# Performance work log

Measured on AMD Instinct MI355X. Metric: run time of the kernel, lower is better.

Reference implementation:

```python
import jax, jax.numpy as jnp
import numpy as np
from jax.scipy.linalg import expm

B, T, D = 4096, 256, 64


def setup_inputs() -> dict:
    key = jax.random.key(0)
    k1, k2, k3 = jax.random.split(key, 3)
    inputs = jax.random.normal(k1, (B, T, D), dtype=jnp.float32)
    time = jax.random.uniform(k2, (T,), dtype=jnp.float32)  # TIME grid in [0,1)
    kernel = jax.random.normal(k3, (D, D), dtype=jnp.float32) * 0.1  # learned Koopman generator
    return {"inputs": inputs, "time": time, "kernel": kernel}


def reference(inputs, time, kernel):
    # expm(kernel * t) for every t, batched instead of a Python loop: [T, D, D]
    mats = jax.vmap(lambda t: expm(kernel * t))(time)
    # original: einsum('ijk,lk->lij', mats, inputs[:, 0, :]) -> [B, T, D]
    x0 = inputs[:, 0, :]  # [B, D] initial condition
    trajs = jnp.einsum('tij,bj->bti', mats, x0)
    return trajs
```

## Files before the change

kernel.cpp:

```cpp
#include <hip/hip_runtime.h>
#include <math.h>


#define TT 256
#define DD 64
#define BB 4096
#define S1 68
#define THETA 0.5f
#define MTERMS 10

__device__ __forceinline__ void mm68(const float* __restrict__ Lt,
                                     const float* __restrict__ R,
                                     float* __restrict__ C,
                                     float f, float* __restrict__ Eacc, int tid) {
    const int i0 = (tid & 15) * 4;
    const int j0 = (tid >> 4) * 4;
    float acc[4][4];
#pragma unroll
    for (int r = 0; r < 4; ++r)
#pragma unroll
        for (int c = 0; c < 4; ++c) acc[r][c] = 0.f;

#pragma unroll 8
    for (int k = 0; k < 64; ++k) {
        const float4 a = *reinterpret_cast<const float4*>(&Lt[k * S1 + i0]);
        const float4 b = *reinterpret_cast<const float4*>(&R[k * S1 + j0]);
        const float av[4] = {a.x, a.y, a.z, a.w};
        const float bv[4] = {b.x, b.y, b.z, b.w};
#pragma unroll
        for (int r = 0; r < 4; ++r)
#pragma unroll
            for (int c = 0; c < 4; ++c) acc[r][c] = fmaf(av[r], bv[c], acc[r][c]);
    }

#pragma unroll
    for (int r = 0; r < 4; ++r) {
        float4 v;
        v.x = acc[r][0] * f; v.y = acc[r][1] * f; v.z = acc[r][2] * f; v.w = acc[r][3] * f;
        *reinterpret_cast<float4*>(&C[(i0 + r) * S1 + j0]) = v;
        if (Eacc) {
            float* e = &Eacc[(i0 + r) * S1 + j0];
            e[0] += v.x; e[1] += v.y; e[2] += v.z; e[3] += v.w;
        }
    }
}

__device__ __forceinline__ void transpose68(const float* __restrict__ X,
                                            float* __restrict__ XT, int tid) {
    const int i = tid >> 2;
    const int j0 = (tid & 3) * 16;
#pragma unroll
    for (int c4 = 0; c4 < 4; ++c4) {
        const float4 v = *reinterpret_cast<const float4*>(&X[i * S1 + j0 + 4 * c4]);
        XT[(j0 + 4 * c4 + 0) * S1 + i] = v.x;
        XT[(j0 + 4 * c4 + 1) * S1 + i] = v.y;
        XT[(j0 + 4 * c4 + 2) * S1 + i] = v.z;
        XT[(j0 + 4 * c4 + 3) * S1 + i] = v.w;
    }
}

__global__ __launch_bounds__(256)
void expm_kernel(const float* __restrict__ K, const float* __restrict__ tim,
                 float* __restrict__ G) {
    __shared__ float As[64 * S1];
    __shared__ float Pa[64 * S1];
    __shared__ float Pb[64 * S1];
    __shared__ float Et[64 * S1];
    __shared__ float Tx[64 * S1];
    __shared__ float red[64];

    const int tid = threadIdx.x;
    const int t = blockIdx.x;
    const float tval = tim[t];

    if (tid < 64) {
        float s = 0.f;
        for (int j = 0; j < 64; ++j) s += fabsf(K[tid * 64 + j]);
        red[tid] = s;
    }
    __syncthreads();
    if (tid == 0) {
        float m = 0.f;
        for (int i = 0; i < 64; ++i) m = fmaxf(m, red[i]);
        const float nt = m * tval;
        int s = 0;
        if (nt > THETA) {
            s = (int)ceilf(log2f(nt / THETA));
            if (s < 0) s = 0;
        }
        red[0] = ldexpf(tval, -s);
        red[1] = (float)s;
    }
    __syncthreads();
    const float scale = red[0];
    const int sq = (int)red[1];
    __syncthreads();

    {
        const int i = tid >> 2;
        const int j0 = (tid & 3) * 16;
#pragma unroll
        for (int c = 0; c < 16; ++c) {
            const int j = j0 + c;
            const float v = K[i * 64 + j] * scale;
            As[i * S1 + j] = v;
            Pa[j * S1 + i] = v;
            Et[j * S1 + i] = v + ((i == j) ? 1.f : 0.f);
        }
    }
    __syncthreads();

    float* Pcur = Pa;
    float* Pnext = Pb;
    for (int n = 2; n <= MTERMS; ++n) {
        mm68(As, Pcur, Pnext, 1.0f / (float)n, Et, tid);
        __syncthreads();
        float* tmp = Pcur; Pcur = Pnext; Pnext = tmp;
    }

    transpose68(Et, Tx, tid);
    __syncthreads();
    float* cur = Tx;
    float* nxt = Pa;
    const float* curT = Et;
    for (int r = 0; r < sq; ++r) {
        if (r > 0) {
            transpose68(cur, Pb, tid);
            __syncthreads();
            curT = Pb;
        }
        mm68(curT, cur, nxt, 1.f, nullptr, tid);
        __syncthreads();
        float* tmp = cur; cur = nxt; nxt = tmp;
    }

    {
        const int j = tid >> 2;
        const int i0 = (tid & 3) * 16;
        float* outp = G + (size_t)t * 4096 + j * 64 + i0;
#pragma unroll
        for (int c4 = 0; c4 < 4; ++c4) {
            float4 v;
            v.x = cur[(i0 + 4 * c4 + 0) * S1 + j];
            v.y = cur[(i0 + 4 * c4 + 1) * S1 + j];
            v.z = cur[(i0 + 4 * c4 + 2) * S1 + j];
            v.w = cur[(i0 + 4 * c4 + 3) * S1 + j];
            *reinterpret_cast<float4*>(outp + 4 * c4) = v;
        }
    }
}

__global__ __launch_bounds__(256)
void traj_kernel(const float* __restrict__ inputs, const float* __restrict__ G,
                 float* __restrict__ out) {
    __shared__ float MT[64 * 64];
    __shared__ float X0T[64 * S1];

    const int tid = threadIdx.x;
    const int t = blockIdx.x & (TT - 1);
    const int b0 = (blockIdx.x >> 8) * 64;

    {
        const float4* src = reinterpret_cast<const float4*>(G) + (size_t)t * 1024;
        float4* dst = reinterpret_cast<float4*>(MT);
#pragma unroll
        for (int c = 0; c < 4; ++c) dst[tid + 256 * c] = src[tid + 256 * c];
    }
    {
        const int bb = tid >> 2;
        const int j0 = (tid & 3) * 16;
        const float* src = inputs + (size_t)(b0 + bb) * (TT * DD) + j0;
#pragma unroll
        for (int c4 = 0; c4 < 4; ++c4) {
            const float4 v = *reinterpret_cast<const float4*>(src + 4 * c4);
            X0T[(j0 + 4 * c4 + 0) * S1 + bb] = v.x;
            X0T[(j0 + 4 * c4 + 1) * S1 + bb] = v.y;
            X0T[(j0 + 4 * c4 + 2) * S1 + bb] = v.z;
            X0T[(j0 + 4 * c4 + 3) * S1 + bb] = v.w;
        }
    }
    __syncthreads();

    const int n0 = (tid & 15) * 4;
    const int m0 = (tid >> 4) * 4;
    float acc[4][4];
#pragma unroll
    for (int r = 0; r < 4; ++r)
#pragma unroll
        for (int c = 0; c < 4; ++c) acc[r][c] = 0.f;

#pragma unroll 8
    for (int k = 0; k < 64; ++k) {
        const float4 a = *reinterpret_cast<const float4*>(&X0T[k * S1 + m0]);
        const float4 b = *reinterpret_cast<const float4*>(&MT[k * 64 + n0]);
        const float av[4] = {a.x, a.y, a.z, a.w};
        const float bv[4] = {b.x, b.y, b.z, b.w};
#pragma unroll
        for (int r = 0; r < 4; ++r)
#pragma unroll
            for (int c = 0; c < 4; ++c) acc[r][c] = fmaf(av[r], bv[c], acc[r][c]);
    }

    float* dst = out + (size_t)(b0 + m0) * (TT * DD) + (size_t)t * DD + n0;
#pragma unroll
    for (int r = 0; r < 4; ++r) {
        float4 v;
        v.x = acc[r][0]; v.y = acc[r][1]; v.z = acc[r][2]; v.w = acc[r][3];
        *reinterpret_cast<float4*>(dst + (size_t)r * (TT * DD)) = v;
    }
}

extern "C" void kernel_launch(void* const* d_in, const int* in_sizes, int n_in,
                              void* d_out, int out_size, void* d_ws, size_t ws_size,
                              hipStream_t stream) {
    const float* inputs = (const float*)d_in[0];
    const float* tim    = (const float*)d_in[1];
    const float* K      = (const float*)d_in[2];
    float* out = (float*)d_out;
    float* G   = (float*)d_ws;

    expm_kernel<<<TT, 256, 0, stream>>>(K, tim, G);
    traj_kernel<<<(BB / 64) * TT, 256, 0, stream>>>(inputs, G, out);
}
```

Before: 479.1 us.

## Use split-bf16 MFMA for trajectory GEMM and store expm output untransposed

Replaces the FP32 scalar-FMA trajectory GEMM with MFMA 16x16x32 bf16 instructions. Each fp32 operand is split into a high and a low bf16 part, and three MFMAs per tile (hi*hi, hi*lo, lo*hi) keep accuracy close to fp32. The expm kernel now writes G row-major so both operands load with the same layout. The cost is extra split arithmetic and shared memory, plus slightly reduced precision. The output stores are now scalar and strided rather than float4, on a kernel that is mainly bound by output writes.

```diff
diff --git a/kernel.cpp b/kernel.cpp
--- a/kernel.cpp
+++ b/kernel.cpp
@@ -6,8 +6,13 @@
 #define DD 64
 #define BB 4096
 #define S1 68
+#define LD 72
 #define THETA 0.5f
 #define MTERMS 10
+
+typedef __attribute__((ext_vector_type(8))) short short8;
+typedef __attribute__((ext_vector_type(4))) float f32x4;
+
 
 __device__ __forceinline__ void mm68(const float* __restrict__ Lt,
                                      const float* __restrict__ R,
@@ -135,78 +140,91 @@
     }
 
     {
-        const int j = tid >> 2;
-        const int i0 = (tid & 3) * 16;
-        float* outp = G + (size_t)t * 4096 + j * 64 + i0;
+        const int i = tid >> 2;
+        const int j0 = (tid & 3) * 16;
+        float* outp = G + (size_t)t * 4096 + i * 64 + j0;
 #pragma unroll
         for (int c4 = 0; c4 < 4; ++c4) {
-            float4 v;
-            v.x = cur[(i0 + 4 * c4 + 0) * S1 + j];
-            v.y = cur[(i0 + 4 * c4 + 1) * S1 + j];
-            v.z = cur[(i0 + 4 * c4 + 2) * S1 + j];
-            v.w = cur[(i0 + 4 * c4 + 3) * S1 + j];
-            *reinterpret_cast<float4*>(outp + 4 * c4) = v;
-        }
-    }
+            *reinterpret_cast<float4*>(outp + 4 * c4) =
+                *reinterpret_cast<const float4*>(&cur[i * S1 + j0 + 4 * c4]);
+        }
+    }
+}
+
+
+__device__ __forceinline__ void bf16_split(float x, unsigned short& hi, unsigned short& lo) {
+    union { float f; unsigned int u; } a; a.f = x;
+    unsigned int r = (a.u + 0x7fffu + ((a.u >> 16) & 1u)) & 0xffff0000u;
+    hi = (unsigned short)(r >> 16);
+    union { float f; unsigned int u; } d; d.f = x - __uint_as_float(r);
+    lo = (unsigned short)(d.u >> 16);
 }
 
 __global__ __launch_bounds__(256)
-void traj_kernel(const float* __restrict__ inputs, const float* __restrict__ G,
-                 float* __restrict__ out) {
-    __shared__ float MT[64 * 64];
-    __shared__ float X0T[64 * S1];
+void traj_mfma(const float* __restrict__ inputs, const float* __restrict__ G,
+               float* __restrict__ out) {
+    __shared__ unsigned short Ahi[64 * LD];
+    __shared__ unsigned short Alo[64 * LD];
+    __shared__ unsigned short Bhi[64 * LD];
+    __shared__ unsigned short Blo[64 * LD];
 
     const int tid = threadIdx.x;
-    const int t = blockIdx.x & (TT - 1);
+    const int t  = blockIdx.x & (TT - 1);
     const int b0 = (blockIdx.x >> 8) * 64;
 
     {
-        const float4* src = reinterpret_cast<const float4*>(G) + (size_t)t * 1024;
-        float4* dst = reinterpret_cast<float4*>(MT);
-#pragma unroll
-        for (int c = 0; c < 4; ++c) dst[tid + 256 * c] = src[tid + 256 * c];
-    }
-    {
-        const int bb = tid >> 2;
-        const int j0 = (tid & 3) * 16;
-        const float* src = inputs + (size_t)(b0 + bb) * (TT * DD) + j0;
-#pragma unroll
-        for (int c4 = 0; c4 < 4; ++c4) {
-            const float4 v = *reinterpret_cast<const float4*>(src + 4 * c4);
-            X0T[(j0 + 4 * c4 + 0) * S1 + bb] = v.x;
-            X0T[(j0 + 4 * c4 + 1) * S1 + bb] = v.y;
-            X0T[(j0 + 4 * c4 + 2) * S1 + bb] = v.z;
-            X0T[(j0 + 4 * c4 + 3) * S1 + bb] = v.w;
-        }
-    }
-    __syncthreads();
-
-    const int n0 = (tid & 15) * 4;
-    const int m0 = (tid >> 4) * 4;
-    float acc[4][4];
-#pragma unroll
-    for (int r = 0; r < 4; ++r)
-#pragma unroll
-        for (int c = 0; c < 4; ++c) acc[r][c] = 0.f;
-
-#pragma unroll 8
-    for (int k = 0; k < 64; ++k) {
-        const float4 a = *reinterpret_cast<const float4*>(&X0T[k * S1 + m0]);
-        const float4 b = *reinterpret_cast<const float4*>(&MT[k * 64 + n0]);
-        const float av[4] = {a.x, a.y, a.z, a.w};
-        const float bv[4] = {b.x, b.y, b.z, b.w};
-#pragma unroll
-        for (int r = 0; r < 4; ++r)
-#pragma unroll
-            for (int c = 0; c < 4; ++c) acc[r][c] = fmaf(av[r], bv[c], acc[r][c]);
-    }
-
-    float* dst = out + (size_t)(b0 + m0) * (TT * DD) + (size_t)t * DD + n0;
+        const int row  = tid >> 2;
+        const int col0 = (tid & 3) * 16;
+        const float* asrc = inputs + (size_t)(b0 + row) * (TT * DD) + col0;
+        const float* bsrc = G + (size_t)t * 4096 + row * 64 + col0;
+#pragma unroll
+        for (int c = 0; c < 4; ++c) {
+            const float4 va = *reinterpret_cast<const float4*>(asrc + 4 * c);
+            const float4 vb = *reinterpret_cast<const float4*>(bsrc + 4 * c);
+            ushort4 ah, al, bh, bl;
+            bf16_split(va.x, ah.x, al.x); bf16_split(va.y, ah.y, al.y);
+            bf16_split(va.z, ah.z, al.z); bf16_split(va.w, ah.w, al.w);
+            bf16_split(vb.x, bh.x, bl.x); bf16_split(vb.y, bh.y, bl.y);
+            bf16_split(vb.z, bh.z, bl.z); bf16_split(vb.w, bh.w, bl.w);
+            const int o = row * LD + col0 + 4 * c;
+            *reinterpret_cast<ushort4*>(&Ahi[o]) = ah;
+            *reinterpret_cast<ushort4*>(&Alo[o]) = al;
+            *reinterpret_cast<ushort4*>(&Bhi[o]) = bh;
+            *reinterpret_cast<ushort4*>(&Blo[o]) = bl;
+        }
+    }
+    __syncthreads();
+
+    const int w  = tid >> 6;
+    const int ln = tid & 15;
+    const int qd = (tid >> 4) & 3;
+
+    f32x4 acc[4];
+#pragma unroll
+    for (int nt = 0; nt < 4; ++nt) acc[nt] = (f32x4){0.f, 0.f, 0.f, 0.f};
+
+#pragma unroll
+    for (int kh = 0; kh < 2; ++kh) {
+        const int ko = kh * 32 + qd * 8;
+        const short8 ah = *reinterpret_cast<const short8*>(&Ahi[(w * 16 + ln) * LD + ko]);
+        const short8 al = *reinterpret_cast<const short8*>(&Alo[(w * 16 + ln) * LD + ko]);
+#pragma unroll
+        for (int nt = 0; nt < 4; ++nt) {
+            const short8 bh = *reinterpret_cast<const short8*>(&Bhi[(nt * 16 + ln) * LD + ko]);
+            const short8 bl = *reinterpret_cast<const short8*>(&Blo[(nt * 16 + ln) * LD + ko]);
+            acc[nt] = __builtin_amdgcn_mfma_f32_16x16x32_bf16(ah, bh, acc[nt], 0, 0, 0);
+            acc[nt] = __builtin_amdgcn_mfma_f32_16x16x32_bf16(ah, bl, acc[nt], 0, 0, 0);
+            acc[nt] = __builtin_amdgcn_mfma_f32_16x16x32_bf16(al, bh, acc[nt], 0, 0, 0);
+        }
+    }
+
+    float* obase = out + (size_t)(b0 + w * 16 + qd * 4) * (TT * DD) + (size_t)t * DD + ln;
 #pragma unroll
     for (int r = 0; r < 4; ++r) {
-        float4 v;
-        v.x = acc[r][0]; v.y = acc[r][1]; v.z = acc[r][2]; v.w = acc[r][3];
-        *reinterpret_cast<float4*>(dst + (size_t)r * (TT * DD)) = v;
+#pragma unroll
+        for (int nt = 0; nt < 4; ++nt) {
+            obase[(size_t)r * (TT * DD) + nt * 16] = acc[nt][r];
+        }
     }
 }
 
@@ -220,5 +238,5 @@
     float* G   = (float*)d_ws;
 
     expm_kernel<<<TT, 256, 0, stream>>>(K, tim, G);
-    traj_kernel<<<(BB / 64) * TT, 256, 0, stream>>>(inputs, G, out);
-}
+    traj_mfma<<<(BB / 64) * TT, 256, 0, stream>>>(inputs, G, out);
+}
```

New measurement: 440.8 us. 8.0% less time.
